# Performance work log

Hardware: AMD Instinct MI355X
Metric: run time of the kernel (lower is better)

Reference implementation:

```python
import jax, jax.numpy as jnp
import numpy as np

B, N, F_IN = 8, 1024, 64
HEADS = 8
D = F_IN  # out_features per head (in_features == out_features)


def setup_inputs() -> dict:
    key = jax.random.key(0)
    ks = jax.random.split(key, 5)
    stdv = 1.0 / np.sqrt(F_IN * HEADS)
    h = jax.random.normal(ks[0], (B, N, F_IN), dtype=jnp.float32)
    adj = jnp.ones((B, N, N), dtype=jnp.float32)  # passed but unused by the module
    W = jax.random.uniform(ks[1], (F_IN, D * HEADS), minval=-stdv, maxval=stdv, dtype=jnp.float32)
    a = jax.random.uniform(ks[2], (2 * D, 1), minval=-stdv, maxval=stdv, dtype=jnp.float32)
    out_W = jax.random.normal(ks[3], (D * HEADS, F_IN), dtype=jnp.float32) / np.sqrt(D * HEADS)
    out_b = jnp.zeros((F_IN,), dtype=jnp.float32)
    return {"h": h, "adj": adj, "W": W, "a": a, "out_W": out_W, "out_b": out_b}


def reference(h, adj, W, a, out_W, out_b):
    Bv, Nv, _ = h.shape
    Dh = W.shape[1] // HEADS
    # Wh: [B, N, H, D]
    Wh = (h @ W).reshape(Bv, Nv, HEADS, Dh)
    # Additive attention decomposed: e[b,i,j,h] = leaky_relu(Wh[b,i,h].a_src + Wh[b,j,h].a_dst)
    a_src = jnp.einsum('bnhd,d->bnh', Wh, a[:Dh, 0])
    a_dst = jnp.einsum('bnhd,d->bnh', Wh, a[Dh:, 0])
    e = jax.nn.leaky_relu(a_src[:, :, None, :] + a_dst[:, None, :, :], negative_slope=0.01)  # [B,N,N,H]
    # Module applies softmax over dim=1 (the first node axis i)
    attn = jax.nn.softmax(e, axis=1)  # [B,N,N,H]
    # h_prime[b,i,h,:] = sum_j attn[b,i,j,h] * Wh[b,j,h,:]
    h_prime = jnp.einsum('bijh,bjhd->bihd', attn, Wh).reshape(Bv, Nv, HEADS * Dh)
    return h_prime @ out_W + out_b
```

## Files before the change

kernel.cpp:

```cpp
#include <hip/hip_runtime.h>


#define B_  8
#define N_  1024
#define H_  8
#define D_  64
#define BH_ 64
#define CH_ 32
#define CL_ 32

__global__ __launch_bounds__(256) void k_wh(
    const float* __restrict__ h, const float* __restrict__ W,
    const float* __restrict__ a,
    float* __restrict__ Wh, float* __restrict__ sArr, float* __restrict__ tArr) {
  __shared__ float hL[16 * 64];
  __shared__ float whL[16 * 512];
  __shared__ float aL[128];
  const int tid = threadIdx.x;
  const int row0 = blockIdx.x * 16;
  const int b = row0 >> 10;
  for (int i = tid; i < 16 * 64; i += 256) hL[i] = h[row0 * 64 + i];
  if (tid < 128) aL[tid] = a[tid];
  __syncthreads();

  float acc0[16], acc1[16];
#pragma unroll
  for (int r = 0; r < 16; ++r) { acc0[r] = 0.f; acc1[r] = 0.f; }
  for (int k = 0; k < 64; ++k) {
    const float w0 = W[k * 512 + tid];
    const float w1 = W[k * 512 + tid + 256];
#pragma unroll
    for (int r = 0; r < 16; ++r) {
      const float hv = hL[r * 64 + k];
      acc0[r] += hv * w0;
      acc1[r] += hv * w1;
    }
  }
  const int hh0 = tid >> 6, d0 = tid & 63;
  const int hh1 = (tid + 256) >> 6;
#pragma unroll
  for (int r = 0; r < 16; ++r) {
    const int n = (row0 + r) & (N_ - 1);
    whL[r * 512 + tid] = acc0[r];
    whL[r * 512 + tid + 256] = acc1[r];
    Wh[((b * H_ + hh0) * N_ + n) * D_ + d0] = acc0[r];
    Wh[((b * H_ + hh1) * N_ + n) * D_ + d0] = acc1[r];
  }
  __syncthreads();
  if (tid < 128) {
    const int r = tid >> 3, hh = tid & 7;
    const int n = (row0 + r) & (N_ - 1);
    float accS = 0.f, accT = 0.f;
    for (int jj = 0; jj < 64; ++jj) {
      const int d = (jj + tid) & 63;
      const float wv = whL[r * 512 + hh * 64 + d];
      accS += wv * aL[d];
      accT += wv * aL[64 + d];
    }
    sArr[(b * H_ + hh) * N_ + n] = accS;
    tArr[(b * H_ + hh) * N_ + n] = accT;
  }
}

__global__ __launch_bounds__(1024) void k_sort(
    const float* __restrict__ sArr, const float* __restrict__ tArr,
    const float* __restrict__ Wh,
    int* __restrict__ tsi, float* __restrict__ uArr, float* __restrict__ vArr,
    int* __restrict__ qrk,
    float* __restrict__ cOff1, float* __restrict__ cOff2) {
  __shared__ float sL[1024];
  __shared__ float tvL[1024];
  __shared__ int   tiL[1024];
  __shared__ float cum1L[1024], cum001L[1024];
  __shared__ float uL[1024], vL[1024];
  __shared__ float cs1[CH_ * 64], cs2[CH_ * 64];
  __shared__ float ws1[16], ws2[16];
  const int tid = threadIdx.x;
  const int lane = tid & 63;
  const int wv_ = tid >> 6;
  const int bh = blockIdx.x;

  const float orig_s = sArr[bh * N_ + tid];
  float sv_r = orig_s;
  float tv_r = tArr[bh * N_ + tid];
  int   ti_r = tid;

  for (int size = 2; size <= 1024; size <<= 1) {
    for (int stride = size >> 1; stride > 0; stride >>= 1) {
      const bool up = ((tid & size) == 0);
      const bool lower = ((tid & stride) == 0);
      float psv, ptv; int pti;
      if (stride >= 64) {
        sL[tid] = sv_r; tvL[tid] = tv_r; tiL[tid] = ti_r;
        __syncthreads();
        const int p = tid ^ stride;
        psv = sL[p]; ptv = tvL[p]; pti = tiL[p];
        __syncthreads();
      } else {
        psv = __shfl_xor(sv_r, stride);
        ptv = __shfl_xor(tv_r, stride);
        pti = __shfl_xor(ti_r, stride);
      }
      const bool sameDir = (up == lower);
      const bool pLessS = (psv < sv_r);
      if (pLessS == sameDir) sv_r = psv;
      const bool pLessT = (ptv < tv_r) || (ptv == tv_r && pti < ti_r);
      if (pLessT == sameDir) { tv_r = ptv; ti_r = pti; }
    }
  }
  sL[tid] = sv_r; tvL[tid] = tv_r; tiL[tid] = ti_r;

  float c1 = __expf(sv_r) , c001 = __expf(0.01f * sv_r);
  {
    float a1 = c1, a2 = c001;
#pragma unroll
    for (int off = 1; off < 64; off <<= 1) {
      const float x1 = __shfl_up(a1, off);
      const float x2 = __shfl_up(a2, off);
      if (lane >= off) { a1 += x1; a2 += x2; }
    }
    if (lane == 63) { ws1[wv_] = a1; ws2[wv_] = a2; }
    __syncthreads();
    float o1 = 0.f, o2 = 0.f;
    for (int ww = 0; ww < 16; ++ww) {
      if (ww < wv_) { o1 += ws1[ww]; o2 += ws2[ww]; }
    }
    c1 = a1 + o1; c001 = a2 + o2;
  }
  cum1L[tid] = c1; cum001L[tid] = c001;
  __syncthreads();
  const float totalHi = cum1L[1023];

  {
    const float tj = tv_r;
    const float th = -tj;
    int lo = 0, hi = 1024;
    while (lo < hi) { const int mid = (lo + hi) >> 1; if (sL[mid] <= th) lo = mid + 1; else hi = mid; }
    const float S_lo = (lo > 0) ? cum001L[lo - 1] : 0.f;
    const float S_hi = totalHi - ((lo > 0) ? cum1L[lo - 1] : 0.f);
    const float et = __expf(tj), et001 = __expf(0.01f * tj);
    const float Z = et * S_hi + et001 * S_lo;
    const float u = et / Z, v = et001 / Z;
    uL[tid] = u; vL[tid] = v;
    uArr[bh * N_ + tid] = u; vArr[bh * N_ + tid] = v;
    tsi[bh * N_ + tid] = ti_r;
  }

  {
    const float th = -orig_s;
    int lo = 0, hi = 1024;
    while (lo < hi) { const int mid = (lo + hi) >> 1; if (tvL[mid] <= th) lo = mid + 1; else hi = mid; }
    qrk[bh * N_ + tid] = lo;
  }
  __syncthreads();

  const int c = tid >> 6, d = tid & 63;
#pragma unroll
  for (int half = 0; half < 2; ++half) {
    const int cc = c + half * 16;
    float s1 = 0.f, s2 = 0.f;
    for (int k2 = 0; k2 < CL_; ++k2) {
      const int k = cc * CL_ + k2;
      const int j = tiL[k];
      const float w = Wh[(bh * N_ + j) * D_ + d];
      s1 += uL[k] * w;
      s2 += vL[k] * w;
    }
    cs1[cc * 64 + d] = s1; cs2[cc * 64 + d] = s2;
  }
  __syncthreads();
#pragma unroll
  for (int half = 0; half < 2; ++half) {
    const int cc = c + half * 16;
    float o1 = 0.f, o2 = 0.f;
    for (int m = 0; m < cc; ++m) { o1 += cs1[m * 64 + d]; o2 += cs2[m * 64 + d]; }
    cOff1[(bh * CH_ + cc) * 64 + d] = o1;
    cOff2[(bh * CH_ + cc) * 64 + d] = o2;
  }
}

__global__ __launch_bounds__(64) void k_inc(
    const float* __restrict__ Wh, const int* __restrict__ tsi,
    const float* __restrict__ uArr, const float* __restrict__ vArr,
    const float* __restrict__ cOff1, const float* __restrict__ cOff2,
    float* __restrict__ INC1, float* __restrict__ INC2) {
  const int blk = blockIdx.x;
  const int bh = blk >> 5, c = blk & (CH_ - 1);
  const int d = threadIdx.x;
  float r1 = cOff1[blk * 64 + d];
  float r2 = cOff2[blk * 64 + d];
  const int base = bh * N_;
#pragma unroll 8
  for (int k2 = 0; k2 < CL_; ++k2) {
    const int k = c * CL_ + k2;
    const int j = tsi[base + k];
    const float u = uArr[base + k], v = vArr[base + k];
    const float w = Wh[(base + j) * D_ + d];
    r1 += u * w;
    r2 += v * w;
    INC1[(base + k) * D_ + d] = r1;
    INC2[(base + k) * D_ + d] = r2;
  }
}

__global__ __launch_bounds__(512) void k_out(
    const float* __restrict__ sArr, const int* __restrict__ qrk,
    const float* __restrict__ INC1, const float* __restrict__ INC2,
    const float* __restrict__ outW, const float* __restrict__ outb,
    float* __restrict__ out) {
  __shared__ float hpL[16 * 512];
  __shared__ float part[8 * 8 * 64];
  __shared__ int   rkI[16 * 8];
  __shared__ float esL[16 * 8], es001L[16 * 8];
  const int tid = threadIdx.x;
  const int row0 = blockIdx.x * 16;
  const int b = row0 >> 10;

  if (tid < 128) {
    const int r = tid >> 3, hh = tid & 7;
    const int bh = b * H_ + hh;
    const int n = (row0 + r) & (N_ - 1);
    const float si = sArr[bh * N_ + n];
    rkI[tid] = qrk[bh * N_ + n];
    esL[tid] = __expf(si);
    es001L[tid] = __expf(0.01f * si);
  }
  __syncthreads();

  {
    const int hh = tid >> 6, d = tid & 63;
    const int bh = b * H_ + hh;
    const float T1 = INC1[(bh * N_ + (N_ - 1)) * D_ + d];
    for (int r = 0; r < 16; ++r) {
      const int rk = rkI[r * 8 + hh];
      float i1 = 0.f, i2 = 0.f;
      if (rk > 0) {
        i1 = INC1[(bh * N_ + rk - 1) * D_ + d];
        i2 = INC2[(bh * N_ + rk - 1) * D_ + d];
      }
      hpL[r * 512 + hh * 64 + d] =
          esL[r * 8 + hh] * (T1 - i1) + es001L[r * 8 + hh] * i2;
    }
  }
  __syncthreads();

  const int cc = tid & 63, p = tid >> 6;
  float acc[16];
#pragma unroll
  for (int r = 0; r < 16; ++r) acc[r] = 0.f;
  for (int k = p * 64; k < p * 64 + 64; ++k) {
    const float wvv = outW[k * 64 + cc];
#pragma unroll
    for (int r = 0; r < 16; ++r) acc[r] += hpL[r * 512 + k] * wvv;
  }
  for (int half = 0; half < 2; ++half) {
#pragma unroll
    for (int r = 0; r < 8; ++r) part[(p * 8 + r) * 64 + cc] = acc[half * 8 + r];
    __syncthreads();
    {
      const int r = tid >> 6, c2 = tid & 63;
      float ssum = 0.f;
#pragma unroll
      for (int p2 = 0; p2 < 8; ++p2) ssum += part[(p2 * 8 + r) * 64 + c2];
      out[(row0 + half * 8 + r) * 64 + c2] = outb[c2] + ssum;
    }
    __syncthreads();
  }
}

extern "C" void kernel_launch(void* const* d_in, const int* in_sizes, int n_in,
                              void* d_out, int out_size, void* d_ws, size_t ws_size,
                              hipStream_t stream) {
  const float* h    = (const float*)d_in[0];
  const float* W    = (const float*)d_in[2];
  const float* a    = (const float*)d_in[3];
  const float* outW = (const float*)d_in[4];
  const float* outb = (const float*)d_in[5];
  float* out = (float*)d_out;

  float* ws   = (float*)d_ws;
  float* Wh   = ws;
  float* sArr = Wh + (size_t)BH_ * N_ * D_;
  float* tArr = sArr + BH_ * N_;
  int*   tsi  = (int*)(tArr + BH_ * N_);
  float* uArr = (float*)(tsi + BH_ * N_);
  float* vArr = uArr + BH_ * N_;
  int*   qrk  = (int*)(vArr + BH_ * N_);
  float* cOff1 = (float*)(qrk + BH_ * N_);
  float* cOff2 = cOff1 + BH_ * CH_ * 64;
  float* INC1 = cOff2 + BH_ * CH_ * 64;
  float* INC2 = INC1 + (size_t)BH_ * N_ * D_;

  hipLaunchKernelGGL(k_wh,   dim3((B_ * N_) / 16), dim3(256), 0, stream,
                     h, W, a, Wh, sArr, tArr);
  hipLaunchKernelGGL(k_sort, dim3(BH_), dim3(1024), 0, stream,
                     sArr, tArr, Wh, tsi, uArr, vArr, qrk, cOff1, cOff2);
  hipLaunchKernelGGL(k_inc,  dim3(BH_ * CH_), dim3(64), 0, stream,
                     Wh, tsi, uArr, vArr, cOff1, cOff2, INC1, INC2);
  hipLaunchKernelGGL(k_out,  dim3((B_ * N_) / 16), dim3(512), 0, stream,
                     sArr, qrk, INC1, INC2, outW, outb, out);
}
```

Measured before the change: 155.5 us.

## Split output stage into gather and GEMM kernels, read activations as float4

k_wh now reads h rows straight from global memory as float4 instead of staging them in LDS, and unrolls the K loop by four. The final stage is split in two. k_hp gathers the prefix-sum differences into a global hp buffer, and a separate k_gemm does the output projection with float4 loads and a readfirstlane wave index. This removes shared-memory staging and a barrier and raises per-kernel occupancy. The cost is an extra 16MB round trip through global memory for hp plus one more kernel launch.

```diff
diff --git a/kernel.cpp b/kernel.cpp
--- a/kernel.cpp
+++ b/kernel.cpp
@@ -13,27 +13,28 @@
     const float* __restrict__ h, const float* __restrict__ W,
     const float* __restrict__ a,
     float* __restrict__ Wh, float* __restrict__ sArr, float* __restrict__ tArr) {
-  __shared__ float hL[16 * 64];
   __shared__ float whL[16 * 512];
   __shared__ float aL[128];
   const int tid = threadIdx.x;
   const int row0 = blockIdx.x * 16;
   const int b = row0 >> 10;
-  for (int i = tid; i < 16 * 64; i += 256) hL[i] = h[row0 * 64 + i];
   if (tid < 128) aL[tid] = a[tid];
-  __syncthreads();
 
   float acc0[16], acc1[16];
 #pragma unroll
   for (int r = 0; r < 16; ++r) { acc0[r] = 0.f; acc1[r] = 0.f; }
-  for (int k = 0; k < 64; ++k) {
-    const float w0 = W[k * 512 + tid];
-    const float w1 = W[k * 512 + tid + 256];
+  for (int k0 = 0; k0 < 64; k0 += 4) {
+    float w0[4], w1[4];
+#pragma unroll
+    for (int u = 0; u < 4; ++u) {
+      w0[u] = W[(k0 + u) * 512 + tid];
+      w1[u] = W[(k0 + u) * 512 + tid + 256];
+    }
 #pragma unroll
     for (int r = 0; r < 16; ++r) {
-      const float hv = hL[r * 64 + k];
-      acc0[r] += hv * w0;
-      acc1[r] += hv * w1;
+      const float4 hv = *reinterpret_cast<const float4*>(&h[(row0 + r) * 64 + k0]);
+      acc0[r] += hv.x * w0[0] + hv.y * w0[1] + hv.z * w0[2] + hv.w * w0[3];
+      acc1[r] += hv.x * w1[0] + hv.y * w1[1] + hv.z * w1[2] + hv.w * w1[3];
     }
   }
   const int hh0 = tid >> 6, d0 = tid & 63;
@@ -203,13 +204,10 @@
   }
 }
 
-__global__ __launch_bounds__(512) void k_out(
+__global__ __launch_bounds__(512) void k_hp(
     const float* __restrict__ sArr, const int* __restrict__ qrk,
     const float* __restrict__ INC1, const float* __restrict__ INC2,
-    const float* __restrict__ outW, const float* __restrict__ outb,
-    float* __restrict__ out) {
-  __shared__ float hpL[16 * 512];
-  __shared__ float part[8 * 8 * 64];
+    float* __restrict__ hp) {
   __shared__ int   rkI[16 * 8];
   __shared__ float esL[16 * 8], es001L[16 * 8];
   const int tid = threadIdx.x;
@@ -227,42 +225,57 @@
   }
   __syncthreads();
 
-  {
-    const int hh = tid >> 6, d = tid & 63;
-    const int bh = b * H_ + hh;
-    const float T1 = INC1[(bh * N_ + (N_ - 1)) * D_ + d];
+  const int hh = tid >> 6, d = tid & 63;
+  const int bh = b * H_ + hh;
+  const float T1 = INC1[(bh * N_ + (N_ - 1)) * D_ + d];
+#pragma unroll
+  for (int r = 0; r < 16; ++r) {
+    const int rk = rkI[r * 8 + hh];
+    float i1 = 0.f, i2 = 0.f;
+    if (rk > 0) {
+      i1 = INC1[(bh * N_ + rk - 1) * D_ + d];
+      i2 = INC2[(bh * N_ + rk - 1) * D_ + d];
+    }
+    hp[(row0 + r) * 512 + hh * 64 + d] =
+        esL[r * 8 + hh] * (T1 - i1) + es001L[r * 8 + hh] * i2;
+  }
+}
+
+__global__ __launch_bounds__(512) void k_gemm(
+    const float* __restrict__ hp, const float* __restrict__ outW,
+    const float* __restrict__ outb, float* __restrict__ out) {
+  __shared__ float part[8 * 8 * 64];
+  const int tid = threadIdx.x;
+  const int row0 = blockIdx.x * 16;
+  const int cc = tid & 63;
+  const int p = __builtin_amdgcn_readfirstlane(tid >> 6);
+
+  float acc[16];
+#pragma unroll
+  for (int r = 0; r < 16; ++r) acc[r] = 0.f;
+
+  for (int kc = 0; kc < 64; kc += 4) {
+    const int k = p * 64 + kc;
+    float wv[4];
+#pragma unroll
+    for (int u = 0; u < 4; ++u) wv[u] = outW[(k + u) * 64 + cc];
+#pragma unroll
     for (int r = 0; r < 16; ++r) {
-      const int rk = rkI[r * 8 + hh];
-      float i1 = 0.f, i2 = 0.f;
-      if (rk > 0) {
-        i1 = INC1[(bh * N_ + rk - 1) * D_ + d];
-        i2 = INC2[(bh * N_ + rk - 1) * D_ + d];
-      }
-      hpL[r * 512 + hh * 64 + d] =
-          esL[r * 8 + hh] * (T1 - i1) + es001L[r * 8 + hh] * i2;
-    }
-  }
-  __syncthreads();
-
-  const int cc = tid & 63, p = tid >> 6;
-  float acc[16];
-#pragma unroll
-  for (int r = 0; r < 16; ++r) acc[r] = 0.f;
-  for (int k = p * 64; k < p * 64 + 64; ++k) {
-    const float wvv = outW[k * 64 + cc];
-#pragma unroll
-    for (int r = 0; r < 16; ++r) acc[r] += hpL[r * 512 + k] * wvv;
-  }
+      const float4 hv = *reinterpret_cast<const float4*>(&hp[(row0 + r) * 512 + k]);
+      acc[r] += hv.x * wv[0] + hv.y * wv[1] + hv.z * wv[2] + hv.w * wv[3];
+    }
+  }
+
   for (int half = 0; half < 2; ++half) {
 #pragma unroll
     for (int r = 0; r < 8; ++r) part[(p * 8 + r) * 64 + cc] = acc[half * 8 + r];
     __syncthreads();
     {
-      const int r = tid >> 6, c2 = tid & 63;
+      const int r2 = tid >> 6, c2 = tid & 63;
       float ssum = 0.f;
 #pragma unroll
-      for (int p2 = 0; p2 < 8; ++p2) ssum += part[(p2 * 8 + r) * 64 + c2];
-      out[(row0 + half * 8 + r) * 64 + c2] = outb[c2] + ssum;
+      for (int p2 = 0; p2 < 8; ++p2) ssum += part[(p2 * 8 + r2) * 64 + c2];
+      out[(row0 + half * 8 + r2) * 64 + c2] = outb[c2] + ssum;
     }
     __syncthreads();
   }
@@ -290,6 +303,7 @@
   float* cOff2 = cOff1 + BH_ * CH_ * 64;
   float* INC1 = cOff2 + BH_ * CH_ * 64;
   float* INC2 = INC1 + (size_t)BH_ * N_ * D_;
+  float* hp   = INC2 + (size_t)BH_ * N_ * D_;
 
   hipLaunchKernelGGL(k_wh,   dim3((B_ * N_) / 16), dim3(256), 0, stream,
                      h, W, a, Wh, sArr, tArr);
@@ -297,6 +311,8 @@
                      sArr, tArr, Wh, tsi, uArr, vArr, qrk, cOff1, cOff2);
   hipLaunchKernelGGL(k_inc,  dim3(BH_ * CH_), dim3(64), 0, stream,
                      Wh, tsi, uArr, vArr, cOff1, cOff2, INC1, INC2);
-  hipLaunchKernelGGL(k_out,  dim3((B_ * N_) / 16), dim3(512), 0, stream,
-                     sArr, qrk, INC1, INC2, outW, outb, out);
-}
+  hipLaunchKernelGGL(k_hp,   dim3((B_ * N_) / 16), dim3(512), 0, stream,
+                     sArr, qrk, INC1, INC2, hp);
+  hipLaunchKernelGGL(k_gemm, dim3((B_ * N_) / 16), dim3(512), 0, stream,
+                     hp, outW, outb, out);
+}
```

New measurement: 176.3 us. 13.4% more time.
